# Performance work log

Measured on AMD Instinct MI355X. Metric: run time of the kernel, lower is better.

The kernel has to match this reference:

```python
import jax, jax.numpy as jnp
import numpy as np

B, D = 8192, 1024
GATE_BIAS = 0.0
LN_EPS = 1e-5


def _layernorm(x, w, b):
    mu = jnp.mean(x, axis=-1, keepdims=True)
    var = jnp.mean(jnp.square(x - mu), axis=-1, keepdims=True)
    return (x - mu) * jax.lax.rsqrt(var + LN_EPS) * w + b


def setup_inputs() -> dict:
    key = jax.random.key(0)
    ks = jax.random.split(key, 12)
    s_in = 1.0 / np.sqrt(2 * D)  # torch Linear init scale (fan_in = 2*dim)
    return {
        "x": jax.random.normal(ks[0], (B, D), jnp.float32),
        "h": jax.random.normal(ks[1], (B, D), jnp.float32),
        "ln_w": jnp.ones((2 * D,), jnp.float32),
        "ln_b": jnp.zeros((2 * D,), jnp.float32),
        "ln2_w": jnp.ones((2 * D,), jnp.float32),
        "ln2_b": jnp.zeros((2 * D,), jnp.float32),
        "Wg": jax.random.uniform(ks[2], (5 * D, 2 * D), jnp.float32, -s_in, s_in),
        "bg": jax.random.uniform(ks[3], (5 * D,), jnp.float32, -s_in, s_in),
        "Wu": jax.random.uniform(ks[4], (D, 2 * D), jnp.float32, -s_in, s_in),
        "bu": jax.random.uniform(ks[5], (D,), jnp.float32, -s_in, s_in),
    }


def reference(x, h, ln_w, ln_b, ln2_w, ln2_b, Wg, bg, Wu, bu):
    # eval mode: dropout / dropout_mask (ones) / zoneout are identity
    inp = jnp.concatenate([x, h], axis=1)          # [B, 2D]
    inp = _layernorm(inp, ln_w, ln_b)
    gates = inp @ Wg.T + bg                        # [B, 5D]
    g0, g1, g2, g3, g4 = jnp.split(gates, 5, axis=1)
    rx = jax.nn.sigmoid(g0)
    rh = jax.nn.sigmoid(g1)
    z = jax.nn.softmax(jnp.stack([g2, g3, g4 - GATE_BIAS], axis=-1), axis=-1)  # [B, D, 3]
    inp2 = jnp.concatenate([x * rx, h * rh], axis=1)
    inp2 = _layernorm(inp2, ln2_w, ln2_b)
    u = jnp.tanh(inp2 @ Wu.T + bu)                 # [B, D]
    h_new = (jnp.stack([x, h, u], axis=-1) * z).sum(-1)
    return h_new
```

## Files before the change

kernel.cpp:

```cpp
#include <hip/hip_runtime.h>

typedef __attribute__((ext_vector_type(8))) __bf16 bf16x8;
typedef __attribute__((ext_vector_type(4))) float f32x4;

#define B_ROWS 8192
#define D_DIM  1024
#define K_DIM  2048
#define NG     5120

typedef const __attribute__((address_space(1))) void cg_void;
typedef __attribute__((address_space(3))) void lds_void;

__device__ __forceinline__ float bf2f(unsigned short u) {
    union { unsigned int ui; float f; } c; c.ui = ((unsigned int)u) << 16; return c.f;
}
__device__ __forceinline__ unsigned short f2bf(float f) {
    unsigned int u = __float_as_uint(f);
    unsigned int r = u + 0x7fffu + ((u >> 16) & 1u);
    return (unsigned short)(r >> 16);
}
__device__ __forceinline__ float sigm(float v) { return 1.0f / (1.0f + __expf(-v)); }

__global__ __launch_bounds__(256) void cvt_f32_bf16(const float* __restrict__ in,
                                                    unsigned short* __restrict__ out, int n4) {
    int i = blockIdx.x * 256 + threadIdx.x;
    if (i >= n4) return;
    float4 v = reinterpret_cast<const float4*>(in)[i];
    ushort4 o;
    o.x = f2bf(v.x); o.y = f2bf(v.y); o.z = f2bf(v.z); o.w = f2bf(v.w);
    reinterpret_cast<ushort4*>(out)[i] = o;
}

__global__ __launch_bounds__(256) void ln1_kernel(const float* __restrict__ x, const float* __restrict__ h,
                                                  const float* __restrict__ w, const float* __restrict__ b,
                                                  unsigned short* __restrict__ out) {
    const int row = blockIdx.x;
    const int t = threadIdx.x;
    const float4 xv = reinterpret_cast<const float4*>(x + (size_t)row * D_DIM)[t];
    const float4 hv = reinterpret_cast<const float4*>(h + (size_t)row * D_DIM)[t];
    float s  = xv.x + xv.y + xv.z + xv.w + hv.x + hv.y + hv.z + hv.w;
    float s2 = xv.x*xv.x + xv.y*xv.y + xv.z*xv.z + xv.w*xv.w
             + hv.x*hv.x + hv.y*hv.y + hv.z*hv.z + hv.w*hv.w;
#pragma unroll
    for (int off = 32; off > 0; off >>= 1) { s += __shfl_xor(s, off); s2 += __shfl_xor(s2, off); }
    __shared__ float red[8];
    const int wid = t >> 6, lane = t & 63;
    if (lane == 0) { red[wid] = s; red[4 + wid] = s2; }
    __syncthreads();
    s  = red[0] + red[1] + red[2] + red[3];
    s2 = red[4] + red[5] + red[6] + red[7];
    const float mu  = s * (1.0f / K_DIM);
    const float var = s2 * (1.0f / K_DIM) - mu * mu;
    const float inv = rsqrtf(var + 1e-5f);
    const float4 w0 = reinterpret_cast<const float4*>(w)[t];
    const float4 b0 = reinterpret_cast<const float4*>(b)[t];
    const float4 w1 = reinterpret_cast<const float4*>(w + D_DIM)[t];
    const float4 b1 = reinterpret_cast<const float4*>(b + D_DIM)[t];
    ushort4 o0, o1;
    o0.x = f2bf((xv.x - mu) * inv * w0.x + b0.x);
    o0.y = f2bf((xv.y - mu) * inv * w0.y + b0.y);
    o0.z = f2bf((xv.z - mu) * inv * w0.z + b0.z);
    o0.w = f2bf((xv.w - mu) * inv * w0.w + b0.w);
    o1.x = f2bf((hv.x - mu) * inv * w1.x + b1.x);
    o1.y = f2bf((hv.y - mu) * inv * w1.y + b1.y);
    o1.z = f2bf((hv.z - mu) * inv * w1.z + b1.z);
    o1.w = f2bf((hv.w - mu) * inv * w1.w + b1.w);
    reinterpret_cast<ushort4*>(out + (size_t)row * K_DIM)[t] = o0;
    reinterpret_cast<ushort4*>(out + (size_t)row * K_DIM + D_DIM)[t] = o1;
}

__global__ __launch_bounds__(256) void gate_ln2_kernel(const float* __restrict__ x, const float* __restrict__ h,
                                                       const unsigned short* __restrict__ gates,
                                                       const float* __restrict__ w, const float* __restrict__ b,
                                                       unsigned short* __restrict__ out) {
    const int row = blockIdx.x;
    const int t = threadIdx.x;
    const float4 xv = reinterpret_cast<const float4*>(x + (size_t)row * D_DIM)[t];
    const float4 hv = reinterpret_cast<const float4*>(h + (size_t)row * D_DIM)[t];
    const ushort4 g0v = reinterpret_cast<const ushort4*>(gates + (size_t)row * NG)[t];
    const ushort4 g1v = reinterpret_cast<const ushort4*>(gates + (size_t)row * NG + D_DIM)[t];
    float a0 = xv.x * sigm(bf2f(g0v.x));
    float a1 = xv.y * sigm(bf2f(g0v.y));
    float a2 = xv.z * sigm(bf2f(g0v.z));
    float a3 = xv.w * sigm(bf2f(g0v.w));
    float c0 = hv.x * sigm(bf2f(g1v.x));
    float c1 = hv.y * sigm(bf2f(g1v.y));
    float c2 = hv.z * sigm(bf2f(g1v.z));
    float c3 = hv.w * sigm(bf2f(g1v.w));
    float s  = a0 + a1 + a2 + a3 + c0 + c1 + c2 + c3;
    float s2 = a0*a0 + a1*a1 + a2*a2 + a3*a3 + c0*c0 + c1*c1 + c2*c2 + c3*c3;
#pragma unroll
    for (int off = 32; off > 0; off >>= 1) { s += __shfl_xor(s, off); s2 += __shfl_xor(s2, off); }
    __shared__ float red[8];
    const int wid = t >> 6, lane = t & 63;
    if (lane == 0) { red[wid] = s; red[4 + wid] = s2; }
    __syncthreads();
    s  = red[0] + red[1] + red[2] + red[3];
    s2 = red[4] + red[5] + red[6] + red[7];
    const float mu  = s * (1.0f / K_DIM);
    const float var = s2 * (1.0f / K_DIM) - mu * mu;
    const float inv = rsqrtf(var + 1e-5f);
    const float4 w0 = reinterpret_cast<const float4*>(w)[t];
    const float4 b0 = reinterpret_cast<const float4*>(b)[t];
    const float4 w1 = reinterpret_cast<const float4*>(w + D_DIM)[t];
    const float4 b1 = reinterpret_cast<const float4*>(b + D_DIM)[t];
    ushort4 o0, o1;
    o0.x = f2bf((a0 - mu) * inv * w0.x + b0.x);
    o0.y = f2bf((a1 - mu) * inv * w0.y + b0.y);
    o0.z = f2bf((a2 - mu) * inv * w0.z + b0.z);
    o0.w = f2bf((a3 - mu) * inv * w0.w + b0.w);
    o1.x = f2bf((c0 - mu) * inv * w1.x + b1.x);
    o1.y = f2bf((c1 - mu) * inv * w1.y + b1.y);
    o1.z = f2bf((c2 - mu) * inv * w1.z + b1.z);
    o1.w = f2bf((c3 - mu) * inv * w1.w + b1.w);
    reinterpret_cast<ushort4*>(out + (size_t)row * K_DIM)[t] = o0;
    reinterpret_cast<ushort4*>(out + (size_t)row * K_DIM + D_DIM)[t] = o1;
}

#define PH(BUF, H, KQ, LOADB, STAGE_CODE, VMCNT_CODE) do {                                            \
    bf16x8 aF[4];                                                                                     \
    _Pragma("unroll")                                                                                 \
    for (int m = 0; m < 4; ++m)                                                                       \
        aF[m] = *reinterpret_cast<const bf16x8*>(                                                     \
            &smem[((BUF) * 2 + (H)) * 8192 + ((aRdS[m] ^ ((KQ) * 64)) >> 1)]);                        \
    if (LOADB) {                                                                                      \
        _Pragma("unroll")                                                                             \
        for (int n = 0; n < 4; ++n)                                                                   \
            bF[KQ][n] = *reinterpret_cast<const bf16x8*>(                                             \
                &smem[32768 + ((BUF) * 2 + bHalf) * 8192 + ((bRdS[n] ^ ((KQ) * 64)) >> 1)]);          \
    }                                                                                                 \
    STAGE_CODE;                                                                                       \
    VMCNT_CODE;                                                                                       \
    asm volatile("" ::: "memory");                                                                    \
    __builtin_amdgcn_s_barrier();                                                                     \
    asm volatile("" ::: "memory");                                                                    \
    __builtin_amdgcn_s_setprio(1);                                                                    \
    _Pragma("unroll")                                                                                 \
    for (int m = 0; m < 4; ++m)                                                                       \
        _Pragma("unroll")                                                                             \
        for (int n = 0; n < 4; ++n)                                                                   \
            acc[(H) * 4 + m][n] =                                                                     \
                __builtin_amdgcn_mfma_f32_16x16x32_bf16(aF[m], bF[KQ][n], acc[(H) * 4 + m][n], 0, 0, 0);\
    __builtin_amdgcn_s_setprio(0);                                                                    \
    asm volatile("" ::: "memory");                                                                    \
    __builtin_amdgcn_s_barrier();                                                                     \
    asm volatile("" ::: "memory");                                                                    \
} while (0)

#define VMC4 asm volatile("s_waitcnt vmcnt(4)" ::: "memory")
#define NOVM (void)0

__global__ __launch_bounds__(512, 2) void gemm_gates8(const unsigned short* __restrict__ A,
                                                      const unsigned short* __restrict__ W,
                                                      const float* __restrict__ bias,
                                                      unsigned short* __restrict__ C) {
    constexpr int K = K_DIM;
    constexpr int NT = K / 64;
    constexpr int NI = NT / 2;
    extern __shared__ unsigned short smem[];

    const int tid = threadIdx.x;
    const int bid = blockIdx.x;
    const int swz = (bid & 7) * 80 + (bid >> 3);
    const int tm = swz / 20;
    const int tn = swz % 20;
    const int Arow0 = tm * 256;
    const int Brow0 = tn * 256;

    const int lane = tid & 63;
    const int wid = tid >> 6;
    const int wr = wid >> 2;
    const int wc = wid & 3;
    const int fr = lane & 15;
    const int kb = lane >> 4;
    const int bHalf = wc >> 1;
    const int swzl = (fr & 7) << 4;

    int aRdS[4], bRdS[4];
#pragma unroll
    for (int m = 0; m < 4; ++m)
        aRdS[m] = (((wr * 64 + m * 16 + fr) * 128) + kb * 16) ^ swzl;
#pragma unroll
    for (int n = 0; n < 4; ++n)
        bRdS[n] = ((((wc & 1) * 64 + n * 16 + fr) * 128) + kb * 16) ^ swzl;

    size_t aSrc[2], bSrc[2];
    int ldsDst[2];
#pragma unroll
    for (int l = 0; l < 2; ++l) {
        const int off = (l * 512 + tid) * 16;
        const int r = off >> 7;
        const int offS = off ^ ((r & 7) << 4);
        const int cb = (offS & 127) >> 1;
        aSrc[l] = (size_t)(Arow0 + r) * K + cb;
        bSrc[l] = (size_t)(Brow0 + r) * K + cb;
        ldsDst[l] = (l * 512 + tid) * 8;
    }

    auto stageA = [&](int buf, int half, int kt) {
#pragma unroll
        for (int l = 0; l < 2; ++l)
            __builtin_amdgcn_global_load_lds(
                (cg_void*)(A + aSrc[l] + (size_t)half * 128 * K + kt * 64),
                (lds_void*)(&smem[(buf * 2 + half) * 8192 + ldsDst[l]]), 16, 0, 0);
    };
    auto stageB = [&](int buf, int half, int kt) {
#pragma unroll
        for (int l = 0; l < 2; ++l)
            __builtin_amdgcn_global_load_lds(
                (cg_void*)(W + bSrc[l] + (size_t)half * 128 * K + kt * 64),
                (lds_void*)(&smem[32768 + (buf * 2 + half) * 8192 + ldsDst[l]]), 16, 0, 0);
    };

    f32x4 acc[8][4] = {};

    stageA(0, 0, 0); stageA(0, 1, 0); stageB(0, 0, 0); stageB(0, 1, 0);
    stageB(1, 0, 1); stageB(1, 1, 1);
    VMC4;
    asm volatile("" ::: "memory");
    __builtin_amdgcn_s_barrier();
    asm volatile("" ::: "memory");

    for (int i = 0; i < NI; ++i) {
        const int t1 = 2 * i + 1;
        const int t2 = (2 * i + 2) & (NT - 1);
        const int t3 = (2 * i + 3) & (NT - 1);
        bf16x8 bF[2][4];
        PH(0, 0, 0, 1, { stageA(1, 0, t1); stageA(1, 1, t1); }, NOVM);
        PH(0, 0, 1, 1, ;, NOVM);
        PH(0, 1, 0, 0, { stageA(0, 0, t2); }, NOVM);
        PH(0, 1, 1, 0, { stageB(0, 0, t2); }, VMC4);
        PH(1, 0, 0, 1, { stageA(0, 1, t2); stageB(0, 1, t2); }, NOVM);
        PH(1, 0, 1, 1, ;, NOVM);
        PH(1, 1, 0, 0, { stageB(1, 0, t3); }, NOVM);
        PH(1, 1, 1, 0, { stageB(1, 1, t3); }, VMC4);
    }

    const int crowBase = Arow0 + wr * 64;
    const int ccol = Brow0 + wc * 64;
#pragma unroll
    for (int n = 0; n < 4; ++n) {
        const int c = ccol + n * 16 + fr;
        const float bvv = bias[c];
#pragma unroll
        for (int hh = 0; hh < 2; ++hh)
#pragma unroll
            for (int m = 0; m < 4; ++m) {
                const size_t r0 = (size_t)crowBase + hh * 128 + m * 16 + kb * 4;
#pragma unroll
                for (int j = 0; j < 4; ++j)
                    C[(r0 + j) * NG + c] = f2bf(acc[hh * 4 + m][n][j] + bvv);
            }
    }
}

__global__ __launch_bounds__(256) void gemm_out(const unsigned short* __restrict__ A,
                                                const unsigned short* __restrict__ W,
                                                const float* __restrict__ bias,
                                                const unsigned short* __restrict__ gates,
                                                const float* __restrict__ x, const float* __restrict__ h,
                                                float* __restrict__ out) {
    constexpr int K = K_DIM, N = D_DIM;
    __shared__ __attribute__((aligned(16))) unsigned short As[2][128 * 32];
    __shared__ __attribute__((aligned(16))) unsigned short Bs[2][128 * 32];
    const int tid = threadIdx.x;
    const int bid = blockIdx.x;
    const int swz = (bid & 7) * 64 + (bid >> 3);
    const int tn = swz & 7;
    const int tm = swz >> 3;
    const size_t arow0 = (size_t)tm * 128;
    const size_t brow0 = (size_t)tn * 128;

    const int lane = tid & 63;
    const int wid = tid >> 6;
    const int wr = wid >> 1, wc = wid & 1;
    const int fr = lane & 15;
    const int kb = lane >> 4;
    const int aoff = (wr * 64 + fr) * 32 + kb * 8;
    const int boff = (wc * 64 + fr) * 32 + kb * 8;

    f32x4 acc[4][4] = {};

    auto stage = [&](int buf, int k0) {
#pragma unroll
        for (int r = 0; r < 2; ++r) {
            const int idx = r * 256 + tid;
            __builtin_amdgcn_global_load_lds(
                (cg_void*)(A + (arow0 + (idx >> 2)) * K + k0 + (idx & 3) * 8),
                (lds_void*)(&As[buf][idx * 8]), 16, 0, 0);
        }
#pragma unroll
        for (int r = 0; r < 2; ++r) {
            const int idx = r * 256 + tid;
            __builtin_amdgcn_global_load_lds(
                (cg_void*)(W + (brow0 + (idx >> 2)) * K + k0 + (idx & 3) * 8),
                (lds_void*)(&Bs[buf][idx * 8]), 16, 0, 0);
        }
    };

    stage(0, 0);
    __syncthreads();
    int cur = 0;
    constexpr int NT = K / 32;
    for (int t = 0; t < NT; ++t) {
        if (t + 1 < NT) stage(cur ^ 1, (t + 1) * 32);
        bf16x8 af[4], bv[4];
#pragma unroll
        for (int m = 0; m < 4; ++m) af[m] = *reinterpret_cast<const bf16x8*>(&As[cur][aoff + m * 512]);
#pragma unroll
        for (int n = 0; n < 4; ++n) bv[n] = *reinterpret_cast<const bf16x8*>(&Bs[cur][boff + n * 512]);
#pragma unroll
        for (int m = 0; m < 4; ++m)
#pragma unroll
            for (int n = 0; n < 4; ++n)
                acc[m][n] = __builtin_amdgcn_mfma_f32_16x16x32_bf16(af[m], bv[n], acc[m][n], 0, 0, 0);
        __syncthreads();
        cur ^= 1;
    }

    const size_t crow0 = arow0 + wr * 64;
    const int ccol0 = (int)brow0 + wc * 64;
#pragma unroll
    for (int n = 0; n < 4; ++n) {
        const int c = ccol0 + n * 16 + fr;
        const float bvv = bias[c];
#pragma unroll
        for (int m = 0; m < 4; ++m) {
            const size_t r0 = crow0 + m * 16 + kb * 4;
#pragma unroll
            for (int j = 0; j < 4; ++j) {
                const size_t r = r0 + j;
                const float u = tanhf(acc[m][n][j] + bvv);
                const size_t gb = r * NG + c;
                const float g2 = bf2f(gates[gb + 2 * D_DIM]);
                const float g3 = bf2f(gates[gb + 3 * D_DIM]);
                const float g4 = bf2f(gates[gb + 4 * D_DIM]);
                const float mx = fmaxf(fmaxf(g2, g3), g4);
                const float e2 = __expf(g2 - mx), e3 = __expf(g3 - mx), e4 = __expf(g4 - mx);
                const float zi = 1.0f / (e2 + e3 + e4);
                const size_t xi = r * D_DIM + c;
                out[xi] = (x[xi] * e2 + h[xi] * e3 + u * e4) * zi;
            }
        }
    }
}

extern "C" void kernel_launch(void* const* d_in, const int* in_sizes, int n_in,
                              void* d_out, int out_size, void* d_ws, size_t ws_size,
                              hipStream_t stream) {
    const float* x    = (const float*)d_in[0];
    const float* h    = (const float*)d_in[1];
    const float* ln_w = (const float*)d_in[2];
    const float* ln_b = (const float*)d_in[3];
    const float* ln2_w= (const float*)d_in[4];
    const float* ln2_b= (const float*)d_in[5];
    const float* Wg   = (const float*)d_in[6];
    const float* bg   = (const float*)d_in[7];
    const float* Wu   = (const float*)d_in[8];
    const float* bu   = (const float*)d_in[9];
    float* out = (float*)d_out;

    char* ws = (char*)d_ws;
    unsigned short* inp   = (unsigned short*)(ws);
    unsigned short* Wg_b  = (unsigned short*)(ws + 33554432);
    unsigned short* Wu_b  = (unsigned short*)(ws + 33554432 + 20971520);
    unsigned short* gates = (unsigned short*)(ws + 33554432 + 20971520 + 4194304);

    (void)hipFuncSetAttribute((const void*)gemm_gates8,
                              hipFuncAttributeMaxDynamicSharedMemorySize, 131072);

    cvt_f32_bf16<<<(5120 * 2048 / 4 + 255) / 256, 256, 0, stream>>>(Wg, Wg_b, 5120 * 2048 / 4);
    cvt_f32_bf16<<<(1024 * 2048 / 4 + 255) / 256, 256, 0, stream>>>(Wu, Wu_b, 1024 * 2048 / 4);
    ln1_kernel<<<8192, 256, 0, stream>>>(x, h, ln_w, ln_b, inp);
    gemm_gates8<<<640, 512, 131072, stream>>>(inp, Wg_b, bg, gates);
    gate_ln2_kernel<<<8192, 256, 0, stream>>>(x, h, gates, ln2_w, ln2_b, inp);
    gemm_out<<<512, 256, 0, stream>>>(inp, Wu_b, bu, gates, x, h, out);
}
```

Baseline: 331.6 us.

## Run gates GEMM with 512 blocks looping extra tiles; fuse weight conversions

The gates GEMM launches 512 blocks instead of 640; the first 128 blocks process a second tile in a loop, with a full vmcnt drain and barrier between tiles. This is meant to avoid a partial second wave of block launches when only two 128KB-LDS blocks fit per CU. The two weight fp32-to-bf16 conversion launches are merged into one kernel to remove a launch. The tail work still exists, so the critical path is not shortened much, and tile-to-block locality changes.

After: 329.0 us. Within noise of the previous version (-0.8%).

```diff
diff --git a/kernel.cpp b/kernel.cpp
--- a/kernel.cpp
+++ b/kernel.cpp
@@ -21,14 +21,23 @@
 }
 __device__ __forceinline__ float sigm(float v) { return 1.0f / (1.0f + __expf(-v)); }
 
-__global__ __launch_bounds__(256) void cvt_f32_bf16(const float* __restrict__ in,
-                                                    unsigned short* __restrict__ out, int n4) {
+__global__ __launch_bounds__(256) void cvt2_f32_bf16(const float* __restrict__ wg,
+                                                     const float* __restrict__ wu,
+                                                     unsigned short* __restrict__ og,
+                                                     unsigned short* __restrict__ ou) {
+    const int NG4 = 5120 * 2048 / 4;
+    const int NU4 = 1024 * 2048 / 4;
     int i = blockIdx.x * 256 + threadIdx.x;
-    if (i >= n4) return;
-    float4 v = reinterpret_cast<const float4*>(in)[i];
-    ushort4 o;
-    o.x = f2bf(v.x); o.y = f2bf(v.y); o.z = f2bf(v.z); o.w = f2bf(v.w);
-    reinterpret_cast<ushort4*>(out)[i] = o;
+    if (i < NG4) {
+        float4 v = reinterpret_cast<const float4*>(wg)[i];
+        ushort4 o; o.x = f2bf(v.x); o.y = f2bf(v.y); o.z = f2bf(v.z); o.w = f2bf(v.w);
+        reinterpret_cast<ushort4*>(og)[i] = o;
+    } else if (i < NG4 + NU4) {
+        int j = i - NG4;
+        float4 v = reinterpret_cast<const float4*>(wu)[j];
+        ushort4 o; o.x = f2bf(v.x); o.y = f2bf(v.y); o.z = f2bf(v.z); o.w = f2bf(v.w);
+        reinterpret_cast<ushort4*>(ou)[j] = o;
+    }
 }
 
 __global__ __launch_bounds__(256) void ln1_kernel(const float* __restrict__ x, const float* __restrict__ h,
@@ -148,6 +157,7 @@
 } while (0)
 
 #define VMC4 asm volatile("s_waitcnt vmcnt(4)" ::: "memory")
+#define VMC0 asm volatile("s_waitcnt vmcnt(0)" ::: "memory")
 #define NOVM (void)0
 
 __global__ __launch_bounds__(512, 2) void gemm_gates8(const unsigned short* __restrict__ A,
@@ -161,12 +171,6 @@
 
     const int tid = threadIdx.x;
     const int bid = blockIdx.x;
-    const int swz = (bid & 7) * 80 + (bid >> 3);
-    const int tm = swz / 20;
-    const int tn = swz % 20;
-    const int Arow0 = tm * 256;
-    const int Brow0 = tn * 256;
-
     const int lane = tid & 63;
     const int wid = tid >> 6;
     const int wr = wid >> 2;
@@ -184,73 +188,93 @@
     for (int n = 0; n < 4; ++n)
         bRdS[n] = ((((wc & 1) * 64 + n * 16 + fr) * 128) + kb * 16) ^ swzl;
 
-    size_t aSrc[2], bSrc[2];
-    int ldsDst[2];
+    int srcRow[2], srcCol[2], ldsDst[2];
 #pragma unroll
     for (int l = 0; l < 2; ++l) {
         const int off = (l * 512 + tid) * 16;
         const int r = off >> 7;
         const int offS = off ^ ((r & 7) << 4);
-        const int cb = (offS & 127) >> 1;
-        aSrc[l] = (size_t)(Arow0 + r) * K + cb;
-        bSrc[l] = (size_t)(Brow0 + r) * K + cb;
+        srcRow[l] = r;
+        srcCol[l] = (offS & 127) >> 1;
         ldsDst[l] = (l * 512 + tid) * 8;
     }
 
-    auto stageA = [&](int buf, int half, int kt) {
-#pragma unroll
-        for (int l = 0; l < 2; ++l)
-            __builtin_amdgcn_global_load_lds(
-                (cg_void*)(A + aSrc[l] + (size_t)half * 128 * K + kt * 64),
-                (lds_void*)(&smem[(buf * 2 + half) * 8192 + ldsDst[l]]), 16, 0, 0);
-    };
-    auto stageB = [&](int buf, int half, int kt) {
-#pragma unroll
-        for (int l = 0; l < 2; ++l)
-            __builtin_amdgcn_global_load_lds(
-                (cg_void*)(W + bSrc[l] + (size_t)half * 128 * K + kt * 64),
-                (lds_void*)(&smem[32768 + (buf * 2 + half) * 8192 + ldsDst[l]]), 16, 0, 0);
-    };
-
-    f32x4 acc[8][4] = {};
-
-    stageA(0, 0, 0); stageA(0, 1, 0); stageB(0, 0, 0); stageB(0, 1, 0);
-    stageB(1, 0, 1); stageB(1, 1, 1);
-    VMC4;
-    asm volatile("" ::: "memory");
-    __builtin_amdgcn_s_barrier();
-    asm volatile("" ::: "memory");
-
-    for (int i = 0; i < NI; ++i) {
-        const int t1 = 2 * i + 1;
-        const int t2 = (2 * i + 2) & (NT - 1);
-        const int t3 = (2 * i + 3) & (NT - 1);
-        bf16x8 bF[2][4];
-        PH(0, 0, 0, 1, { stageA(1, 0, t1); stageA(1, 1, t1); }, NOVM);
-        PH(0, 0, 1, 1, ;, NOVM);
-        PH(0, 1, 0, 0, { stageA(0, 0, t2); }, NOVM);
-        PH(0, 1, 1, 0, { stageB(0, 0, t2); }, VMC4);
-        PH(1, 0, 0, 1, { stageA(0, 1, t2); stageB(0, 1, t2); }, NOVM);
-        PH(1, 0, 1, 1, ;, NOVM);
-        PH(1, 1, 0, 0, { stageB(1, 0, t3); }, NOVM);
-        PH(1, 1, 1, 0, { stageB(1, 1, t3); }, VMC4);
-    }
-
-    const int crowBase = Arow0 + wr * 64;
-    const int ccol = Brow0 + wc * 64;
-#pragma unroll
-    for (int n = 0; n < 4; ++n) {
-        const int c = ccol + n * 16 + fr;
-        const float bvv = bias[c];
-#pragma unroll
-        for (int hh = 0; hh < 2; ++hh)
-#pragma unroll
-            for (int m = 0; m < 4; ++m) {
-                const size_t r0 = (size_t)crowBase + hh * 128 + m * 16 + kb * 4;
-#pragma unroll
-                for (int j = 0; j < 4; ++j)
-                    C[(r0 + j) * NG + c] = f2bf(acc[hh * 4 + m][n][j] + bvv);
-            }
+    const int nrep = (bid < 128) ? 2 : 1;
+    for (int rep = 0; rep < nrep; ++rep) {
+        const int tile = bid + rep * 512;
+        const int swz = (tile & 7) * 80 + (tile >> 3);
+        const int tm = swz / 20;
+        const int tn = swz % 20;
+        const int Arow0 = tm * 256;
+        const int Brow0 = tn * 256;
+
+        size_t aSrc[2], bSrc[2];
+#pragma unroll
+        for (int l = 0; l < 2; ++l) {
+            aSrc[l] = (size_t)(Arow0 + srcRow[l]) * K + srcCol[l];
+            bSrc[l] = (size_t)(Brow0 + srcRow[l]) * K + srcCol[l];
+        }
+
+        auto stageA = [&](int buf, int half, int kt) {
+#pragma unroll
+            for (int l = 0; l < 2; ++l)
+                __builtin_amdgcn_global_load_lds(
+                    (cg_void*)(A + aSrc[l] + (size_t)half * 128 * K + kt * 64),
+                    (lds_void*)(&smem[(buf * 2 + half) * 8192 + ldsDst[l]]), 16, 0, 0);
+        };
+        auto stageB = [&](int buf, int half, int kt) {
+#pragma unroll
+            for (int l = 0; l < 2; ++l)
+                __builtin_amdgcn_global_load_lds(
+                    (cg_void*)(W + bSrc[l] + (size_t)half * 128 * K + kt * 64),
+                    (lds_void*)(&smem[32768 + (buf * 2 + half) * 8192 + ldsDst[l]]), 16, 0, 0);
+        };
+
+        f32x4 acc[8][4] = {};
+
+        stageA(0, 0, 0); stageA(0, 1, 0); stageB(0, 0, 0); stageB(0, 1, 0);
+        stageB(1, 0, 1); stageB(1, 1, 1);
+        VMC4;
+        asm volatile("" ::: "memory");
+        __builtin_amdgcn_s_barrier();
+        asm volatile("" ::: "memory");
+
+        for (int i = 0; i < NI; ++i) {
+            const int t1 = 2 * i + 1;
+            const int t2 = (2 * i + 2) & (NT - 1);
+            const int t3 = (2 * i + 3) & (NT - 1);
+            bf16x8 bF[2][4];
+            PH(0, 0, 0, 1, { stageA(1, 0, t1); stageA(1, 1, t1); }, NOVM);
+            PH(0, 0, 1, 1, ;, NOVM);
+            PH(0, 1, 0, 0, { stageA(0, 0, t2); }, NOVM);
+            PH(0, 1, 1, 0, { stageB(0, 0, t2); }, VMC4);
+            PH(1, 0, 0, 1, { stageA(0, 1, t2); stageB(0, 1, t2); }, NOVM);
+            PH(1, 0, 1, 1, ;, NOVM);
+            PH(1, 1, 0, 0, { stageB(1, 0, t3); }, NOVM);
+            PH(1, 1, 1, 0, { stageB(1, 1, t3); }, VMC4);
+        }
+
+        VMC0;
+        asm volatile("" ::: "memory");
+        __builtin_amdgcn_s_barrier();
+        asm volatile("" ::: "memory");
+
+        const int crowBase = Arow0 + wr * 64;
+        const int ccol = Brow0 + wc * 64;
+#pragma unroll
+        for (int n = 0; n < 4; ++n) {
+            const int c = ccol + n * 16 + fr;
+            const float bvv = bias[c];
+#pragma unroll
+            for (int hh = 0; hh < 2; ++hh)
+#pragma unroll
+                for (int m = 0; m < 4; ++m) {
+                    const size_t r0 = (size_t)crowBase + hh * 128 + m * 16 + kb * 4;
+#pragma unroll
+                    for (int j = 0; j < 4; ++j)
+                        C[(r0 + j) * NG + c] = f2bf(acc[hh * 4 + m][n][j] + bvv);
+                }
+        }
     }
 }
 
@@ -369,10 +393,10 @@
     (void)hipFuncSetAttribute((const void*)gemm_gates8,
                               hipFuncAttributeMaxDynamicSharedMemorySize, 131072);
 
-    cvt_f32_bf16<<<(5120 * 2048 / 4 + 255) / 256, 256, 0, stream>>>(Wg, Wg_b, 5120 * 2048 / 4);
-    cvt_f32_bf16<<<(1024 * 2048 / 4 + 255) / 256, 256, 0, stream>>>(Wu, Wu_b, 1024 * 2048 / 4);
+    const int nCvt4 = 5120 * 2048 / 4 + 1024 * 2048 / 4;
+    cvt2_f32_bf16<<<(nCvt4 + 255) / 256, 256, 0, stream>>>(Wg, Wu, Wg_b, Wu_b);
     ln1_kernel<<<8192, 256, 0, stream>>>(x, h, ln_w, ln_b, inp);
-    gemm_gates8<<<640, 512, 131072, stream>>>(inp, Wg_b, bg, gates);
+    gemm_gates8<<<512, 512, 131072, stream>>>(inp, Wg_b, bg, gates);
     gate_ln2_kernel<<<8192, 256, 0, stream>>>(x, h, gates, ln2_w, ln2_b, inp);
     gemm_out<<<512, 256, 0, stream>>>(inp, Wu_b, bu, gates, x, h, out);
 }
```
